# Performance work log

Measured on AMD Instinct MI355X. Metric: run time of the kernel, lower is better.

## Reference

```python
import jax, jax.numpy as jnp
import numpy as np

B, S, D = 2, 2048, 4096
H, KVH, DH = 32, 8, 128
KVD = KVH * DH  # 1024
EPS = 1e-6
SCALING = DH ** -0.5


def _rms_norm(x, scale):
    xf = x.astype(jnp.float32)
    var = jnp.mean(xf * xf, axis=-1, keepdims=True)
    return (xf * jax.lax.rsqrt(var + EPS)).astype(x.dtype) * scale


def _rotate_half(x):
    half = x.shape[-1] // 2
    return jnp.concatenate([-x[..., half:], x[..., :half]], axis=-1)


def setup_inputs() -> dict:
    key = jax.random.key(0)
    ks = jax.random.split(key, 5)
    hidden_states = jax.random.normal(ks[0], (B, S, D), dtype=jnp.float32)
    w_qkv = jax.random.normal(ks[1], (D, D + 2 * KVD), dtype=jnp.float32) * 0.02
    w_out = jax.random.normal(ks[2], (D, D), dtype=jnp.float32) * 0.02
    q_scale = jnp.ones((D,), dtype=jnp.float32)
    k_scale = jnp.ones((KVD,), dtype=jnp.float32)
    # real rotary tables: cos/sin of positions, broadcast to batch
    inv_freq = 1.0 / (10000.0 ** (np.arange(0, DH, 2, dtype=np.float32) / DH))
    pos = np.arange(S, dtype=np.float32)
    freqs = np.outer(pos, inv_freq)            # [S, DH/2]
    emb = np.concatenate([freqs, freqs], -1)   # [S, DH]
    cos_cached = jnp.broadcast_to(jnp.asarray(np.cos(emb)), (B, S, DH))
    sin_cached = jnp.broadcast_to(jnp.asarray(np.sin(emb)), (B, S, DH))
    # causal mask: True = masked
    idx = jnp.arange(S)
    attention_mask = (idx[None, :] > idx[:, None])[None, None].repeat(B, 0)  # [B,1,S,S] bool
    return {
        "hidden_states": hidden_states, "w_qkv": w_qkv, "w_out": w_out,
        "q_scale": q_scale, "k_scale": k_scale,
        "cos_cached": cos_cached, "sin_cached": sin_cached,
        "attention_mask": attention_mask,
    }


def reference(hidden_states, w_qkv, w_out, q_scale, k_scale, cos_cached, sin_cached, attention_mask):
    b, s, _ = hidden_states.shape
    qkv = jnp.einsum("bsd,de->bse", hidden_states, w_qkv)
    q, k, v = jnp.split(qkv, [D, D + KVD], axis=-1)
    # qk-norm applied pre-view over full projected dim (non-qwen3 path)
    q = _rms_norm(q, q_scale)
    k = _rms_norm(k, k_scale)
    q = q.reshape(b, s, H, DH).transpose(0, 2, 1, 3)    # [B,H,S,DH]
    k = k.reshape(b, s, KVH, DH).transpose(0, 2, 1, 3)  # [B,KVH,S,DH]
    v = v.reshape(b, s, KVH, DH).transpose(0, 2, 1, 3)
    cos = cos_cached[:, None]  # [B,1,S,DH]
    sin = sin_cached[:, None]
    q = q * cos + _rotate_half(q) * sin
    k = k * cos + _rotate_half(k) * sin
    # repeat KV heads to match query heads (GQA)
    n_rep = H // KVH
    k = jnp.repeat(k, n_rep, axis=1)
    v = jnp.repeat(v, n_rep, axis=1)
    scores = jnp.einsum("bhsd,bhtd->bhst", q, k) * SCALING
    scores = jnp.where(attention_mask, jnp.float32(-10000.0), scores)
    attn = jax.nn.softmax(scores.astype(jnp.float32), axis=-1).astype(q.dtype)
    out = jnp.einsum("bhst,bhtd->bhsd", attn, v)
    out = out.transpose(0, 2, 1, 3).reshape(b, s, H * DH)
    return jnp.einsum("bsd,de->bse", out, w_out)
```

## Files before the change

### kernel.cpp

```cpp
#include <hip/hip_runtime.h>
#include <hip/hip_bf16.h>
#include <cstdint>
#include <cstddef>

#define BB 2
#define SS 2048
#define DD 4096
#define HH 32
#define KVH 8
#define DH 128
#define KVD 1024
#define SCALE 0.08838834764831845f
#define QSC 0.1275178745225f

typedef __attribute__((ext_vector_type(8))) short short8;
typedef __attribute__((ext_vector_type(4))) float f32x4;

typedef __attribute__((address_space(1))) void GV;
typedef __attribute__((address_space(3))) void LV;

__device__ __forceinline__ void async16(const void* g, void* l) {
  __builtin_amdgcn_global_load_lds((GV*)g, (LV*)l, 16, 0, 0);
}

__device__ __forceinline__ unsigned short f2bf(float x) {
  union { float f; uint32_t u; } v; v.f = x;
  uint32_t r = (v.u + 0x7fffu + ((v.u >> 16) & 1u)) >> 16;
  return (unsigned short)r;
}
__device__ __forceinline__ float bf2f(unsigned short b) {
  union { uint32_t u; float f; } v; v.u = ((uint32_t)b) << 16; return v.f;
}
__device__ __forceinline__ f32x4 mfma16(short8 a, short8 b, f32x4 c) {
  return __builtin_amdgcn_mfma_f32_16x16x32_bf16(a, b, c, 0, 0, 0);
}

__global__ __launch_bounds__(256) void cast_bf16_kernel(
    const float* __restrict__ in, unsigned short* __restrict__ out, int n4) {
  int i = blockIdx.x * 256 + threadIdx.x;
  if (i >= n4) return;
  float4 v = ((const float4*)in)[i];
  ushort4 o;
  o.x = f2bf(v.x); o.y = f2bf(v.y); o.z = f2bf(v.z); o.w = f2bf(v.w);
  ((ushort4*)out)[i] = o;
}

__global__ __launch_bounds__(256) void transpose_cast_kernel(
    const float* __restrict__ in, unsigned short* __restrict__ out, int R, int C) {
  __shared__ unsigned short tile[32][33];
  const int tx = threadIdx.x, ty = threadIdx.y;
  const int c0 = blockIdx.x * 32, r0 = blockIdx.y * 32;
  for (int i = ty; i < 32; i += 8)
    tile[i][tx] = f2bf(in[(size_t)(r0 + i) * C + c0 + tx]);
  __syncthreads();
  for (int i = ty; i < 32; i += 8)
    out[(size_t)(c0 + i) * R + r0 + tx] = tile[tx][i];
}

__global__ __launch_bounds__(256) void transpose_v_kernel(
    const unsigned short* __restrict__ qkv, unsigned short* __restrict__ vo) {
  __shared__ unsigned short tile[32][33];
  const int s0 = blockIdx.x * 32, d0 = blockIdx.y * 32;
  const int b = blockIdx.z >> 3, kvh = blockIdx.z & 7;
  const int tx = threadIdx.x, ty = threadIdx.y;
  const unsigned short* ip = qkv + 5120 + (size_t)kvh * 128 + d0 + tx;
  for (int i = ty; i < 32; i += 8)
    tile[i][tx] = ip[(size_t)(b * SS + s0 + i) * 6144];
  __syncthreads();
  unsigned short* op = vo + (size_t)(b * KVH + kvh) * DH * SS + s0 + tx;
  for (int i = ty; i < 32; i += 8)
    op[(size_t)(d0 + i) * SS] = tile[tx][i];
}


#define GBAR()  asm volatile("s_barrier" ::: "memory")
#define GLGKM0()                                              \
  do {                                                        \
    asm volatile("s_waitcnt lgkmcnt(0)" ::: "memory");        \
    __builtin_amdgcn_sched_barrier(0);                        \
  } while (0)

#define STG_A(tt, mh, p)                                                         \
  do {                                                                           \
    async16(Abase + (size_t)(arb0 + (mh) * 64) * K + (size_t)(tt) * 64 + loffA,  \
            ldsA + (p) * 16384 + (arb0 + (mh) * 64) * 64);                       \
    async16(Abase + (size_t)(arb1 + (mh) * 64) * K + (size_t)(tt) * 64 + loffA,  \
            ldsA + (p) * 16384 + (arb1 + (mh) * 64) * 64);                       \
  } while (0)
#define STG_B(tt, nh, p)                                                         \
  do {                                                                           \
    async16(Bbase + (size_t)(brb0 + (nh) * 32) * K + (size_t)(tt) * 64 + loffB,  \
            ldsB + (p) * 16384 + (brb0 + (nh) * 32) * 64);                       \
    async16(Bbase + (size_t)(brb1 + (nh) * 32) * K + (size_t)(tt) * 64 + loffB,  \
            ldsB + (p) * 16384 + (brb1 + (nh) * 32) * 64);                       \
  } while (0)

template <typename OutT>
__global__ __launch_bounds__(512, 2) void gemm_bt(
    const unsigned short* __restrict__ A, const unsigned short* __restrict__ Bt,
    OutT* __restrict__ C, int M, int N, int K) {
  __shared__ __align__(16) unsigned short lds[65536];
  unsigned short* ldsA = lds;
  unsigned short* ldsB = lds + 32768;
  const int tid = threadIdx.x;
  const int wave = __builtin_amdgcn_readfirstlane(tid >> 6);
  const int lane = tid & 63, quad = lane >> 4, l16 = lane & 15;

  const int tn_n = N >> 8;
  const int nwg = (int)gridDim.x;
  const int q = nwg >> 3, r = nwg & 7;
  const int xcd = (int)blockIdx.x & 7, lin = (int)blockIdx.x >> 3;
  const int wg = (xcd < r) ? xcd * (q + 1) + lin
                           : r * (q + 1) + (xcd - r) * q + lin;
  const int m0 = (wg / tn_n) * 256, n0 = (wg % tn_n) * 256;

  const int blk0 = wave * 2, blk1 = blk0 + 1;
  const int arb0 = ((blk0 & 7) << 3) + ((blk0 >> 3) << 7);
  const int arb1 = ((blk1 & 7) << 3) + ((blk1 >> 3) << 7);
  const int brb0 = ((blk0 >> 2) << 6) + ((blk0 & 3) << 3);
  const int brb1 = ((blk1 >> 2) << 6) + ((blk1 & 3) << 3);
  const int lrow = lane >> 3;
  const int loffA = lrow * K + (((lane & 7) ^ lrow) << 3);
  const int loffB = loffA;
  const unsigned short* Abase = A + (size_t)m0 * K;
  const unsigned short* Bbase = Bt + (size_t)n0 * K;

  const int pg0 = ((quad) ^ (l16 & 7)) * 8;
  const int pg1 = ((quad + 4) ^ (l16 & 7)) * 8;
  const int arow = ((wave >> 2) * 128 + l16) * 64;
  const int brow = ((wave & 3) * 64 + l16) * 64;

  f32x4 acc[8][4] = {};
  short8 a0[4], a1[4], bl0[2], bl1[2], bh0[2], bh1[2];

  STG_A(0, 0, 0); STG_B(0, 0, 0); STG_B(0, 1, 0); STG_A(0, 1, 0);
  STG_A(1, 0, 1); STG_B(1, 0, 1); STG_B(1, 1, 1); STG_A(1, 1, 1);
  asm volatile("s_waitcnt vmcnt(8)" ::: "memory");
  GBAR();

  const int nt = K >> 6;
  for (int t = 0; t < nt; ++t) {
    const int p = t & 1;
    const bool st = (t + 2 < nt);
    const unsigned short* pA = ldsA + p * 16384 + arow;
    const unsigned short* pB = ldsB + p * 16384 + brow;

#pragma unroll
    for (int i = 0; i < 4; ++i) {
      a0[i] = *(const short8*)(pA + i * 1024 + pg0);
      a1[i] = *(const short8*)(pA + i * 1024 + pg1);
    }
#pragma unroll
    for (int j = 0; j < 2; ++j) {
      bl0[j] = *(const short8*)(pB + j * 1024 + pg0);
      bl1[j] = *(const short8*)(pB + j * 1024 + pg1);
    }
    GBAR();
    GLGKM0();
    __builtin_amdgcn_s_setprio(1);
#pragma unroll
    for (int i = 0; i < 4; ++i)
#pragma unroll
      for (int j = 0; j < 2; ++j) {
        acc[i][j] = mfma16(a0[i], bl0[j], acc[i][j]);
        acc[i][j] = mfma16(a1[i], bl1[j], acc[i][j]);
      }
    __builtin_amdgcn_sched_barrier(0);
    __builtin_amdgcn_s_setprio(0);
    GBAR();

#pragma unroll
    for (int j = 0; j < 2; ++j) {
      bh0[j] = *(const short8*)(pB + (j + 2) * 1024 + pg0);
      bh1[j] = *(const short8*)(pB + (j + 2) * 1024 + pg1);
    }
    if (st) STG_A(t + 2, 0, p);
    GBAR();
    GLGKM0();
    __builtin_amdgcn_s_setprio(1);
#pragma unroll
    for (int i = 0; i < 4; ++i)
#pragma unroll
      for (int j = 0; j < 2; ++j) {
        acc[i][j + 2] = mfma16(a0[i], bh0[j], acc[i][j + 2]);
        acc[i][j + 2] = mfma16(a1[i], bh1[j], acc[i][j + 2]);
      }
    __builtin_amdgcn_sched_barrier(0);
    __builtin_amdgcn_s_setprio(0);
    GBAR();

#pragma unroll
    for (int i = 0; i < 4; ++i) {
      a0[i] = *(const short8*)(pA + (i + 4) * 1024 + pg0);
      a1[i] = *(const short8*)(pA + (i + 4) * 1024 + pg1);
    }
    if (st) STG_B(t + 2, 0, p);
    GBAR();
    GLGKM0();
    __builtin_amdgcn_s_setprio(1);
#pragma unroll
    for (int i = 0; i < 4; ++i)
#pragma unroll
      for (int j = 0; j < 2; ++j) {
        acc[i + 4][j + 2] = mfma16(a0[i], bh0[j], acc[i + 4][j + 2]);
        acc[i + 4][j + 2] = mfma16(a1[i], bh1[j], acc[i + 4][j + 2]);
      }
    __builtin_amdgcn_sched_barrier(0);
    __builtin_amdgcn_s_setprio(0);
    GBAR();

    if (st) {
      STG_B(t + 2, 1, p);
      STG_A(t + 2, 1, p);
      asm volatile("s_waitcnt vmcnt(8)" ::: "memory");
    } else {
      asm volatile("s_waitcnt vmcnt(0)" ::: "memory");
    }
    GBAR();
    __builtin_amdgcn_s_setprio(1);
#pragma unroll
    for (int i = 0; i < 4; ++i)
#pragma unroll
      for (int j = 0; j < 2; ++j) {
        acc[i + 4][j] = mfma16(a0[i], bl0[j], acc[i + 4][j]);
        acc[i + 4][j] = mfma16(a1[i], bl1[j], acc[i + 4][j]);
      }
    __builtin_amdgcn_sched_barrier(0);
    __builtin_amdgcn_s_setprio(0);
    GBAR();
  }

  const int cm = m0 + (wave >> 2) * 128 + quad * 4;
  const int cn = n0 + (wave & 3) * 64 + l16;
#pragma unroll
  for (int i = 0; i < 8; ++i)
#pragma unroll
    for (int j = 0; j < 4; ++j)
#pragma unroll
      for (int rr = 0; rr < 4; ++rr) {
        const size_t idx = (size_t)(cm + i * 16 + rr) * N + (cn + j * 16);
        if constexpr (sizeof(OutT) == 4) C[idx] = acc[i][j][rr];
        else                             C[idx] = (OutT)f2bf(acc[i][j][rr]);
      }
}

#undef STG_A
#undef STG_B

__global__ __launch_bounds__(256) void rmsnorm_rope_kernel(
    const unsigned short* __restrict__ qkv,
    const float* __restrict__ q_scale, const float* __restrict__ k_scale,
    const float* __restrict__ cosc, const float* __restrict__ sinc,
    unsigned short* __restrict__ qo,
    unsigned short* __restrict__ ko)
{
  const int row = blockIdx.x;
  const int b = row >> 11, s = row & 2047;
  const int tid = threadIdx.x;
  const unsigned short* qr = qkv + (size_t)row * 6144;
  short8 qv0 = *(const short8*)&qr[tid * 8];
  short8 qv1 = *(const short8*)&qr[2048 + tid * 8];
  ushort4 kv = *(const ushort4*)&qr[4096 + tid * 4];
  float sq = 0.f, sk = 0.f;
#pragma unroll
  for (int e = 0; e < 8; e++) {
    float a = bf2f((unsigned short)qv0[e]); sq += a * a;
    float c = bf2f((unsigned short)qv1[e]); sq += c * c;
  }
  float kf[4];
#pragma unroll
  for (int e = 0; e < 4; e++) {
    kf[e] = bf2f(((const unsigned short*)&kv)[e]); sk += kf[e] * kf[e];
  }
#pragma unroll
  for (int off = 32; off; off >>= 1) {
    sq += __shfl_down(sq, off, 64);
    sk += __shfl_down(sk, off, 64);
  }
  __shared__ float redq[4], redk[4];
  if ((tid & 63) == 0) { redq[tid >> 6] = sq; redk[tid >> 6] = sk; }
  __syncthreads();
  sq = redq[0] + redq[1] + redq[2] + redq[3];
  sk = redk[0] + redk[1] + redk[2] + redk[3];
  const float rq = rsqrtf(sq * (1.f / 4096.f) + 1e-6f);
  const float rk = rsqrtf(sk * (1.f / 1024.f) + 1e-6f);
  const float* cp = cosc + (size_t)row * 128;
  const float* sp = sinc + (size_t)row * 128;
#pragma unroll
  for (int it = 0; it < 2; it++) {
    const int c = it * 2048 + tid * 8;
    const int d = c & 127, hh = c >> 7;
    short8 v8 = it ? qv1 : qv0;
    short8 p8 = *(const short8*)&qr[c ^ 64];
    const float sgn = (d < 64) ? -1.f : 1.f;
    ushort o8[8];
#pragma unroll
    for (int e = 0; e < 8; e++) {
      float v = bf2f((unsigned short)v8[e]) * rq * q_scale[c + e];
      float p = bf2f((unsigned short)p8[e]) * rq * q_scale[(c ^ 64) + e];
      o8[e] = f2bf((v * cp[d + e] + sgn * p * sp[d + e]) * QSC);
    }
    *(uint4*)&qo[((size_t)(b * HH + hh) * SS + s) * DH + d] = *(const uint4*)o8;
  }
  {
    const int c = tid * 4;
    const int d = c & 127, hh = c >> 7;
    ushort4 p4 = *(const ushort4*)&qr[4096 + (c ^ 64)];
    const float sgn = (d < 64) ? -1.f : 1.f;
    ushort o4[4];
#pragma unroll
    for (int e = 0; e < 4; e++) {
      float v = kf[e] * rk * k_scale[c + e];
      float p = bf2f(((const unsigned short*)&p4)[e]) * rk * k_scale[(c ^ 64) + e];
      o4[e] = f2bf(v * cp[d + e] + sgn * p * sp[d + e]);
    }
    *(uint2*)&ko[((size_t)(b * KVH + hh) * SS + s) * DH + d] = *(const uint2*)o4;
  }
}

__global__ __launch_bounds__(256, 2) void flash_attn(
    const unsigned short* __restrict__ Q,
    const unsigned short* __restrict__ Kr,
    const unsigned short* __restrict__ Vt,
    unsigned short* __restrict__ O)
{
  __shared__ __align__(16) unsigned short Ks[8192];
  __shared__ __align__(16) unsigned short Vs[8192];
  __shared__ __align__(16) unsigned int   Ps[4][1024];
  const int tid = threadIdx.x, wave = tid >> 6, lane = tid & 63;
  const int quad = lane >> 4, l16 = lane & 15;
  const int bh = blockIdx.x, b = bh >> 5, h = bh & 31;
  const int kvh = h >> 2;
  const int qbase = ((int)gridDim.y - 1 - (int)blockIdx.y) * 128;
  const unsigned short* Qb = Q + (size_t)(b * HH + h) * SS * DH;
  short8 qf[2][4];
#pragma unroll
  for (int mi = 0; mi < 2; mi++) {
    const unsigned short* Qp = Qb + (size_t)(qbase + mi * 64 + wave * 16 + l16) * DH + quad * 8;
#pragma unroll
    for (int c = 0; c < 4; c++) qf[mi][c] = *(const short8*)(Qp + c * 32);
  }
  const unsigned short* Kg = Kr + (size_t)(b * KVH + kvh) * SS * DH;
  const unsigned short* Vg = Vt + (size_t)(b * KVH + kvh) * DH * SS;
  int bK[4], bV[4];
#pragma unroll
  for (int j = 0; j < 4; j++) {
    const int kk = wave * 16 + j * 4 + quad;
    const int gd = l16 ^ ((j * 4 + quad) & 15);
    bK[j] = kk * 128 + gd * 8;
    const int dd = (wave * 4 + j) * 8 + (lane >> 3);
    const int gk = (lane & 7) ^ ((lane >> 3) & 7);
    bV[j] = dd * 2048 + gk * 8;
  }
  f32x4 o[2][8] = {};
  float m_i[2] = {-1e30f, -1e30f}, l_i[2] = {0.f, 0.f};
  const int ndiag = qbase >> 6;
  const int nkt = ndiag + 2;
  for (int kt = 0; kt < nkt; kt++) {
    const int k0 = kt * 64;
    __syncthreads();
#pragma unroll
    for (int j = 0; j < 4; j++) {
      async16(Kg + (size_t)k0 * 128 + bK[j], Ks + (wave * 4 + j) * 512);
      async16(Vg + k0 + bV[j], Vs + (wave * 4 + j) * 512);
    }
    __syncthreads();
    f32x4 st[4][2] = {};
#pragma unroll
    for (int km = 0; km < 4; km++) {
      const unsigned short* krow = Ks + (km * 16 + l16) * 128;
#pragma unroll
      for (int c = 0; c < 4; c++) {
        short8 kf = *(const short8*)(krow + (((c * 4 + quad) ^ l16) * 8));
        st[km][0] = mfma16(kf, qf[0][c], st[km][0]);
        st[km][1] = mfma16(kf, qf[1][c], st[km][1]);
      }
    }
    const bool mtile = (kt >= ndiag);
    float alpha[2];
#pragma unroll
    for (int mi = 0; mi < 2; mi++) {
      if (mtile) {
        const int qg = qbase + mi * 64 + wave * 16 + l16;
#pragma unroll
        for (int km = 0; km < 4; km++)
#pragma unroll
          for (int r = 0; r < 4; r++)
            if (k0 + km * 16 + quad * 4 + r > qg) st[km][mi][r] = -1e4f;
      }
      float tmax = -3e38f;
#pragma unroll
      for (int km = 0; km < 4; km++)
#pragma unroll
        for (int r = 0; r < 4; r++) tmax = fmaxf(tmax, st[km][mi][r]);
      tmax = fmaxf(tmax, __shfl_xor(tmax, 16, 64));
      tmax = fmaxf(tmax, __shfl_xor(tmax, 32, 64));
      const float mn = fmaxf(m_i[mi], tmax);
      alpha[mi] = __builtin_amdgcn_exp2f(m_i[mi] - mn);
      m_i[mi] = mn;
      float rs = 0.f;
#pragma unroll
      for (int km = 0; km < 4; km++)
#pragma unroll
        for (int r = 0; r < 4; r++) {
          float e = __builtin_amdgcn_exp2f(st[km][mi][r] - mn);
          st[km][mi][r] = e;
          rs += e;
        }
      rs += __shfl_xor(rs, 16, 64);
      rs += __shfl_xor(rs, 32, 64);
      l_i[mi] = l_i[mi] * alpha[mi] + rs;
      unsigned int* pw = &Ps[wave][(mi * 16 + l16) * 32 + (quad & 1) * 2];
#pragma unroll
      for (int km = 0; km < 4; km++) {
        const int g = (km * 2 + (quad >> 1)) ^ (l16 & 7);
        float e0 = st[km][mi][0], e1 = st[km][mi][1], e2 = st[km][mi][2], e3 = st[km][mi][3];
        pw[g * 4]     = __builtin_amdgcn_perm(__builtin_bit_cast(unsigned int, e1),
                                              __builtin_bit_cast(unsigned int, e0), 0x07060302u);
        pw[g * 4 + 1] = __builtin_amdgcn_perm(__builtin_bit_cast(unsigned int, e3),
                                              __builtin_bit_cast(unsigned int, e2), 0x07060302u);
      }
    }
    if (__any((alpha[0] != 1.f) || (alpha[1] != 1.f))) {
#pragma unroll
      for (int mi = 0; mi < 2; mi++) {
        float ar[4];
#pragma unroll
        for (int r = 0; r < 4; r++)
          ar[r] = __shfl(alpha[mi], (lane & 48) + quad * 4 + r, 64);
#pragma unroll
        for (int f = 0; f < 8; f++)
#pragma unroll
          for (int r = 0; r < 4; r++) o[mi][f][r] *= ar[r];
      }
    }
#pragma unroll
    for (int kc = 0; kc < 2; kc++) {
      short8 pa[2];
#pragma unroll
      for (int mi = 0; mi < 2; mi++) {
        const int g = (kc * 4 + quad) ^ (l16 & 7);
        uint4 pv4 = *(const uint4*)&Ps[wave][(mi * 16 + l16) * 32 + g * 4];
        pa[mi] = __builtin_bit_cast(short8, pv4);
      }
#pragma unroll
      for (int f = 0; f < 8; f++) {
        const int d = f * 16 + l16;
        short8 vf = *(const short8*)(Vs + d * 64 + (((kc * 4 + quad) ^ (l16 & 7)) * 8));
        o[0][f] = mfma16(pa[0], vf, o[0][f]);
        o[1][f] = mfma16(pa[1], vf, o[1][f]);
      }
    }
  }
  float il[2][4];
#pragma unroll
  for (int mi = 0; mi < 2; mi++)
#pragma unroll
    for (int r = 0; r < 4; r++) {
      float lv = __shfl(l_i[mi], (lane & 48) + quad * 4 + r, 64);
      il[mi][r] = 1.f / lv;
    }
#pragma unroll
  for (int mi = 0; mi < 2; mi++) {
    unsigned short* Op = O + (size_t)(b * SS + qbase + mi * 64 + wave * 16 + quad * 4) * DD + h * DH + l16;
#pragma unroll
    for (int f = 0; f < 8; f++)
#pragma unroll
      for (int r = 0; r < 4; r++)
        Op[(size_t)r * DD + f * 16] = f2bf(o[mi][f][r] * il[mi][r]);
  }
}

extern "C" void kernel_launch(void* const* d_in, const int* in_sizes, int n_in,
                              void* d_out, int out_size, void* d_ws, size_t ws_size,
                              hipStream_t stream) {
  const float* hs      = (const float*)d_in[0];
  const float* wqkv    = (const float*)d_in[1];
  const float* wout    = (const float*)d_in[2];
  const float* q_scale = (const float*)d_in[3];
  const float* k_scale = (const float*)d_in[4];
  const float* cosc    = (const float*)d_in[5];
  const float* sinc    = (const float*)d_in[6];
  float* out = (float*)d_out;

  unsigned short* ws = (unsigned short*)d_ws;
  unsigned short* wqkvT = ws;
  unsigned short* woutT = wqkvT + 25165824;
  unsigned short* hsb   = woutT + 16777216;
  unsigned short* qkv   = hsb + 16777216;
  unsigned short* qrope = wqkvT;
  unsigned short* krope = wqkvT + 16777216;
  unsigned short* vT    = wqkvT + 16777216 + 4194304;
  unsigned short* attno = hsb;

  cast_bf16_kernel<<<16384, 256, 0, stream>>>(hs, hsb, 4194304);
  transpose_cast_kernel<<<dim3(192, 128), dim3(32, 8), 0, stream>>>(wqkv, wqkvT, 4096, 6144);
  transpose_cast_kernel<<<dim3(128, 128), dim3(32, 8), 0, stream>>>(wout, woutT, 4096, 4096);
  gemm_bt<unsigned short><<<dim3(384), 512, 0, stream>>>(hsb, wqkvT, qkv, 4096, 6144, 4096);
  rmsnorm_rope_kernel<<<4096, 256, 0, stream>>>(qkv, q_scale, k_scale, cosc, sinc,
                                                qrope, krope);
  transpose_v_kernel<<<dim3(64, 4, 16), dim3(32, 8), 0, stream>>>(qkv, vT);
  flash_attn<<<dim3(64, 16), 256, 0, stream>>>(qrope, krope, vT, attno);
  gemm_bt<float><<<dim3(256), 512, 0, stream>>>(attno, woutT, out, 4096, 4096, 4096);
}
```

Measured before the change: 752.4 us.

## Software-pipeline LDS fragment loads across GEMM sub-tiles with partial lgkmcnt waits

Restructures the bf16 GEMM main loop so the next k-tile's A0/B0 LDS fragments are issued before the final MFMA quadrant, and the B1/A1 loads overlap the first quadrant. Full lgkmcnt(0) waits become partial waits, several barriers are removed, and the loop is unrolled by two with ping-pong B registers. The aim is to hide LDS read latency behind MFMAs and cut barrier stalls. In exchange it uses more registers, which could affect occupancy under launch bounds (512,2), and it relies on the exact counter values and staging order being correct.

```diff
diff --git a/kernel.cpp b/kernel.cpp
--- a/kernel.cpp
+++ b/kernel.cpp
@@ -74,10 +74,15 @@
 
 
 #define GBAR()  asm volatile("s_barrier" ::: "memory")
-#define GLGKM0()                                              \
-  do {                                                        \
-    asm volatile("s_waitcnt lgkmcnt(0)" ::: "memory");        \
-    __builtin_amdgcn_sched_barrier(0);                        \
+#define WAIT_LGKM(N)                                               \
+  do {                                                             \
+    asm volatile("s_waitcnt lgkmcnt(" #N ")" ::: "memory");        \
+    __builtin_amdgcn_sched_barrier(0);                             \
+  } while (0)
+#define WAIT_VM(N)                                                 \
+  do {                                                             \
+    asm volatile("s_waitcnt vmcnt(" #N ")" ::: "memory");          \
+    __builtin_amdgcn_sched_barrier(0);                             \
   } while (0)
 
 #define STG_A(tt, mh, p)                                                         \
@@ -95,6 +100,85 @@
             ldsB + (p) * 16384 + (brb1 + (nh) * 32) * 64);                       \
   } while (0)
 
+#define ISSUE_A0_B0(P, B0R)                                          \
+  {                                                                  \
+    const unsigned short* pA_ = ldsA + (P) * 16384 + arow;           \
+    const unsigned short* pB_ = ldsB + (P) * 16384 + brow;           \
+    A0[0][0] = *(const short8*)(pA_ + 0 * 1024 + pg0);               \
+    A0[0][1] = *(const short8*)(pA_ + 0 * 1024 + pg1);               \
+    A0[1][0] = *(const short8*)(pA_ + 1 * 1024 + pg0);               \
+    A0[1][1] = *(const short8*)(pA_ + 1 * 1024 + pg1);               \
+    A0[2][0] = *(const short8*)(pA_ + 2 * 1024 + pg0);               \
+    A0[2][1] = *(const short8*)(pA_ + 2 * 1024 + pg1);               \
+    A0[3][0] = *(const short8*)(pA_ + 3 * 1024 + pg0);               \
+    A0[3][1] = *(const short8*)(pA_ + 3 * 1024 + pg1);               \
+    B0R[0][0] = *(const short8*)(pB_ + 0 * 1024 + pg0);              \
+    B0R[0][1] = *(const short8*)(pB_ + 0 * 1024 + pg1);              \
+    B0R[1][0] = *(const short8*)(pB_ + 1 * 1024 + pg0);              \
+    B0R[1][1] = *(const short8*)(pB_ + 1 * 1024 + pg1);              \
+  }
+
+#define ISSUE_B1_A1(P, B1R)                                          \
+  {                                                                  \
+    const unsigned short* pA_ = ldsA + (P) * 16384 + arow;           \
+    const unsigned short* pB_ = ldsB + (P) * 16384 + brow;           \
+    B1R[0][0] = *(const short8*)(pB_ + 2 * 1024 + pg0);              \
+    B1R[0][1] = *(const short8*)(pB_ + 2 * 1024 + pg1);              \
+    B1R[1][0] = *(const short8*)(pB_ + 3 * 1024 + pg0);              \
+    B1R[1][1] = *(const short8*)(pB_ + 3 * 1024 + pg1);              \
+    A1[0][0] = *(const short8*)(pA_ + 4 * 1024 + pg0);               \
+    A1[0][1] = *(const short8*)(pA_ + 4 * 1024 + pg1);               \
+    A1[1][0] = *(const short8*)(pA_ + 5 * 1024 + pg0);               \
+    A1[1][1] = *(const short8*)(pA_ + 5 * 1024 + pg1);               \
+    A1[2][0] = *(const short8*)(pA_ + 6 * 1024 + pg0);               \
+    A1[2][1] = *(const short8*)(pA_ + 6 * 1024 + pg1);               \
+    A1[3][0] = *(const short8*)(pA_ + 7 * 1024 + pg0);               \
+    A1[3][1] = *(const short8*)(pA_ + 7 * 1024 + pg1);               \
+  }
+
+#define QMFMA(I0, J0, AR, BR)                                               \
+  _Pragma("unroll") for (int i_ = 0; i_ < 4; ++i_)                          \
+  _Pragma("unroll") for (int j_ = 0; j_ < 2; ++j_) {                        \
+    acc[(I0) + i_][(J0) + j_] =                                             \
+        mfma16(AR[i_][0], BR[j_][0], acc[(I0) + i_][(J0) + j_]);            \
+    acc[(I0) + i_][(J0) + j_] =                                             \
+        mfma16(AR[i_][1], BR[j_][1], acc[(I0) + i_][(J0) + j_]);            \
+  }
+
+#define BODY(T, P, B0R, B1R)                                                \
+  {                                                                         \
+    const bool st_ = ((T) + 2 < nt);                                        \
+    ISSUE_B1_A1(P, B1R);                                                    \
+    WAIT_LGKM(12);                                         \
+    __builtin_amdgcn_s_setprio(1);                                          \
+    QMFMA(0, 0, A0, B0R);                                                   \
+    __builtin_amdgcn_s_setprio(0);                                          \
+    __builtin_amdgcn_sched_barrier(0);                                      \
+    GBAR();                                   \
+    if (st_) { STG_A((T) + 2, 0, P); STG_B((T) + 2, 0, P); }                \
+    WAIT_LGKM(8);                                             \
+    __builtin_amdgcn_s_setprio(1);                                          \
+    QMFMA(0, 2, A0, B1R);                                                   \
+    __builtin_amdgcn_s_setprio(0);                                          \
+    __builtin_amdgcn_sched_barrier(0);                                      \
+    GBAR();                                        \
+    if (st_) STG_B((T) + 2, 1, P);                                          \
+    WAIT_LGKM(0);                                             \
+    __builtin_amdgcn_s_setprio(1);                                          \
+    QMFMA(4, 2, A1, B1R);                                                   \
+    __builtin_amdgcn_s_setprio(0);                                          \
+    __builtin_amdgcn_sched_barrier(0);                                      \
+    if (st_) { WAIT_VM(6); } else { WAIT_VM(0); }      \
+    GBAR();                                             \
+    if (st_) STG_A((T) + 2, 1, P);                                          \
+    if ((T) + 1 < nt) ISSUE_A0_B0((P) ^ 1, B1R); \
+    __builtin_amdgcn_sched_barrier(0);                                      \
+    __builtin_amdgcn_s_setprio(1);                                          \
+    QMFMA(4, 0, A1, B0R);                                                   \
+    __builtin_amdgcn_s_setprio(0);                                          \
+    __builtin_amdgcn_sched_barrier(0);                                      \
+  }
+
 template <typename OutT>
 __global__ __launch_bounds__(512, 2) void gemm_bt(
     const unsigned short* __restrict__ A, const unsigned short* __restrict__ Bt,
@@ -131,103 +215,18 @@
   const int brow = ((wave & 3) * 64 + l16) * 64;
 
   f32x4 acc[8][4] = {};
-  short8 a0[4], a1[4], bl0[2], bl1[2], bh0[2], bh1[2];
-
+  short8 A0[4][2], A1[4][2], Bx[2][2], By[2][2];
+
+  const int nt = K >> 6;
   STG_A(0, 0, 0); STG_B(0, 0, 0); STG_B(0, 1, 0); STG_A(0, 1, 0);
   STG_A(1, 0, 1); STG_B(1, 0, 1); STG_B(1, 1, 1); STG_A(1, 1, 1);
-  asm volatile("s_waitcnt vmcnt(8)" ::: "memory");
+  WAIT_VM(8);
   GBAR();
-
-  const int nt = K >> 6;
-  for (int t = 0; t < nt; ++t) {
-    const int p = t & 1;
-    const bool st = (t + 2 < nt);
-    const unsigned short* pA = ldsA + p * 16384 + arow;
-    const unsigned short* pB = ldsB + p * 16384 + brow;
-
-#pragma unroll
-    for (int i = 0; i < 4; ++i) {
-      a0[i] = *(const short8*)(pA + i * 1024 + pg0);
-      a1[i] = *(const short8*)(pA + i * 1024 + pg1);
-    }
-#pragma unroll
-    for (int j = 0; j < 2; ++j) {
-      bl0[j] = *(const short8*)(pB + j * 1024 + pg0);
-      bl1[j] = *(const short8*)(pB + j * 1024 + pg1);
-    }
-    GBAR();
-    GLGKM0();
-    __builtin_amdgcn_s_setprio(1);
-#pragma unroll
-    for (int i = 0; i < 4; ++i)
-#pragma unroll
-      for (int j = 0; j < 2; ++j) {
-        acc[i][j] = mfma16(a0[i], bl0[j], acc[i][j]);
-        acc[i][j] = mfma16(a1[i], bl1[j], acc[i][j]);
-      }
-    __builtin_amdgcn_sched_barrier(0);
-    __builtin_amdgcn_s_setprio(0);
-    GBAR();
-
-#pragma unroll
-    for (int j = 0; j < 2; ++j) {
-      bh0[j] = *(const short8*)(pB + (j + 2) * 1024 + pg0);
-      bh1[j] = *(const short8*)(pB + (j + 2) * 1024 + pg1);
-    }
-    if (st) STG_A(t + 2, 0, p);
-    GBAR();
-    GLGKM0();
-    __builtin_amdgcn_s_setprio(1);
-#pragma unroll
-    for (int i = 0; i < 4; ++i)
-#pragma unroll
-      for (int j = 0; j < 2; ++j) {
-        acc[i][j + 2] = mfma16(a0[i], bh0[j], acc[i][j + 2]);
-        acc[i][j + 2] = mfma16(a1[i], bh1[j], acc[i][j + 2]);
-      }
-    __builtin_amdgcn_sched_barrier(0);
-    __builtin_amdgcn_s_setprio(0);
-    GBAR();
-
-#pragma unroll
-    for (int i = 0; i < 4; ++i) {
-      a0[i] = *(const short8*)(pA + (i + 4) * 1024 + pg0);
-      a1[i] = *(const short8*)(pA + (i + 4) * 1024 + pg1);
-    }
-    if (st) STG_B(t + 2, 0, p);
-    GBAR();
-    GLGKM0();
-    __builtin_amdgcn_s_setprio(1);
-#pragma unroll
-    for (int i = 0; i < 4; ++i)
-#pragma unroll
-      for (int j = 0; j < 2; ++j) {
-        acc[i + 4][j + 2] = mfma16(a0[i], bh0[j], acc[i + 4][j + 2]);
-        acc[i + 4][j + 2] = mfma16(a1[i], bh1[j], acc[i + 4][j + 2]);
-      }
-    __builtin_amdgcn_sched_barrier(0);
-    __builtin_amdgcn_s_setprio(0);
-    GBAR();
-
-    if (st) {
-      STG_B(t + 2, 1, p);
-      STG_A(t + 2, 1, p);
-      asm volatile("s_waitcnt vmcnt(8)" ::: "memory");
-    } else {
-      asm volatile("s_waitcnt vmcnt(0)" ::: "memory");
-    }
-    GBAR();
-    __builtin_amdgcn_s_setprio(1);
-#pragma unroll
-    for (int i = 0; i < 4; ++i)
-#pragma unroll
-      for (int j = 0; j < 2; ++j) {
-        acc[i + 4][j] = mfma16(a0[i], bl0[j], acc[i + 4][j]);
-        acc[i + 4][j] = mfma16(a1[i], bl1[j], acc[i + 4][j]);
-      }
-    __builtin_amdgcn_sched_barrier(0);
-    __builtin_amdgcn_s_setprio(0);
-    GBAR();
+  ISSUE_A0_B0(0, Bx);
+
+  for (int t = 0; t < nt; t += 2) {
+    BODY(t, 0, Bx, By);
+    BODY(t + 1, 1, By, Bx);
   }
 
   const int cm = m0 + (wave >> 2) * 128 + quad * 4;
@@ -246,6 +245,10 @@
 
 #undef STG_A
 #undef STG_B
+#undef ISSUE_A0_B0
+#undef ISSUE_B1_A1
+#undef QMFMA
+#undef BODY
 
 __global__ __launch_bounds__(256) void rmsnorm_rope_kernel(
     const unsigned short* __restrict__ qkv,
```

Measured after the change: 725.6 us. 1.04x faster.
